# Kernel optimization log

Measured on AMD Instinct MI355X. Metric: run time of the kernel, lower is better.

## Reference

```python
import jax, jax.numpy as jnp
import numpy as np

EPS = 1e-06


def setup_inputs() -> dict:
    key = jax.random.key(0)
    kq, kk, kv = jax.random.split(key, 3)
    shape = (4, 16, 4096, 64)  # [batch, heads, seq, head_dim]
    q = jax.random.normal(kq, shape, dtype=jnp.float32)
    k = jax.random.normal(kk, shape, dtype=jnp.float32)
    v = jax.random.normal(kv, shape, dtype=jnp.float32)
    return {"q": q, "k": k, "v": v}


def reference(q, k, v):
    # elu(x)+1 feature map (positive kernel)
    q_prime = jax.nn.elu(q) + 1.0  # [b,h,s,d]
    k_prime = jax.nn.elu(k) + 1.0  # [b,h,s,d]
    # KV aggregate: [b,h,d,d] -- avoids the [s,s] score matrix
    kv_agg = jnp.einsum('bhsd,bhse->bhde', k_prime, v)
    num = jnp.einsum('bhsd,bhde->bhse', q_prime, kv_agg)  # [b,h,s,d]
    k_sum = k_prime.sum(axis=-2)                           # [b,h,d]
    denom = jnp.einsum('bhsd,bhd->bhs', q_prime, k_sum)[..., None] + EPS
    return num / denom
```

## Files before the change

### kernel.cpp

```cpp
#include <hip/hip_runtime.h>


#define EPS_LA 1e-6f

constexpr int BH = 64;
constexpr int SEQ = 4096;
constexpr int DIM = 64;
constexpr int KVELEM = DIM * DIM + DIM;
constexpr int NPB = 32;
constexpr int SCH = SEQ / NPB;

typedef short bf16x8 __attribute__((ext_vector_type(8)));
typedef float f32x4 __attribute__((ext_vector_type(4)));

__device__ __forceinline__ float elu1(float x) {
    return x > 0.f ? x + 1.f : __expf(x);
}
__device__ __forceinline__ f32x4 elu4v(f32x4 v) {
    v[0] = elu1(v[0]); v[1] = elu1(v[1]); v[2] = elu1(v[2]); v[3] = elu1(v[3]);
    return v;
}
__device__ __forceinline__ f32x4 ntld(const float* p) {
    return __builtin_nontemporal_load((const f32x4*)p);
}
__device__ __forceinline__ void ntst(float* p, f32x4 v) {
    __builtin_nontemporal_store(v, (f32x4*)p);
}

__device__ __forceinline__ unsigned int f2bf(float x) {
    unsigned int u = __float_as_uint(x);
    return (u + 0x7fffu + ((u >> 16) & 1u)) >> 16;
}
__device__ __forceinline__ unsigned int pack2bf(float lo, float hi) {
    return f2bf(lo) | (f2bf(hi) << 16);
}

__device__ __forceinline__ int swz(int d, int s2) {
    return d * 64 + (s2 ^ ((((d >> 1) ^ (d >> 2)) & 7) << 2));
}

template<bool ATOMIC>
__global__ __launch_bounds__(256, 2) void kv_mfma_kernel(
    const float* __restrict__ K, const float* __restrict__ V,
    float* __restrict__ dst) {
    const int bh = blockIdx.y;
    const int blk = blockIdx.x;
    const int t = threadIdx.x;
    const int w = t >> 6, l = t & 63;

    __shared__ unsigned int KT[64 * 64];
    __shared__ unsigned int VT[64 * 64];
    __shared__ float csumS[4][64];

    const float* Kb = K + ((size_t)bh * SEQ + (size_t)blk * SCH) * DIM;
    const float* Vb = V + ((size_t)bh * SEQ + (size_t)blk * SCH) * DIM;

    const int c0 = (t & 15) * 4;
    const int pg = t >> 4;
    const int lg = l >> 4;
    const int lr = l & 15;

    f32x4 kf[8], vf[8];
    #pragma unroll
    for (int i = 0; i < 4; ++i) {
        const int p = pg + 16 * i;
        kf[2 * i]     = ntld(Kb + (size_t)(2 * p) * DIM + c0);
        kf[2 * i + 1] = ntld(Kb + (size_t)(2 * p + 1) * DIM + c0);
    }
    #pragma unroll
    for (int i = 0; i < 4; ++i) {
        const int p = pg + 16 * i;
        vf[2 * i]     = ntld(Vb + (size_t)(2 * p) * DIM + c0);
        vf[2 * i + 1] = ntld(Vb + (size_t)(2 * p + 1) * DIM + c0);
    }

    float cs0 = 0.f, cs1 = 0.f, cs2 = 0.f, cs3 = 0.f;
    #pragma unroll
    for (int i = 0; i < 4; ++i) {
        const int p = pg + 16 * i;
        const f32x4 ka = elu4v(kf[2 * i]);
        const f32x4 kb = elu4v(kf[2 * i + 1]);
        cs0 += ka[0] + kb[0]; cs1 += ka[1] + kb[1];
        cs2 += ka[2] + kb[2]; cs3 += ka[3] + kb[3];
        KT[swz(c0 + 0, p)] = pack2bf(ka[0], kb[0]);
        KT[swz(c0 + 1, p)] = pack2bf(ka[1], kb[1]);
        KT[swz(c0 + 2, p)] = pack2bf(ka[2], kb[2]);
        KT[swz(c0 + 3, p)] = pack2bf(ka[3], kb[3]);
        const f32x4 va = vf[2 * i], vb = vf[2 * i + 1];
        VT[swz(c0 + 0, p)] = pack2bf(va[0], vb[0]);
        VT[swz(c0 + 1, p)] = pack2bf(va[1], vb[1]);
        VT[swz(c0 + 2, p)] = pack2bf(va[2], vb[2]);
        VT[swz(c0 + 3, p)] = pack2bf(va[3], vb[3]);
    }

    cs0 += __shfl_xor(cs0, 16); cs0 += __shfl_xor(cs0, 32);
    cs1 += __shfl_xor(cs1, 16); cs1 += __shfl_xor(cs1, 32);
    cs2 += __shfl_xor(cs2, 16); cs2 += __shfl_xor(cs2, 32);
    cs3 += __shfl_xor(cs3, 16); cs3 += __shfl_xor(cs3, 32);
    if (l < 16) *(f32x4*)&csumS[w][l * 4] = f32x4{cs0, cs1, cs2, cs3};

    __syncthreads();

    f32x4 acc[4];
    #pragma unroll
    for (int m = 0; m < 4; ++m)
        #pragma unroll
        for (int r = 0; r < 4; ++r) acc[m][r] = 0.f;

    #pragma unroll
    for (int ks = 0; ks < 4; ++ks) {
        const int s2b = ks * 16 + lg * 4;
        const bf16x8 bfrag =
            *reinterpret_cast<const bf16x8*>(&VT[swz(16 * w + lr, s2b)]);
        #pragma unroll
        for (int m = 0; m < 4; ++m) {
            const bf16x8 afrag =
                *reinterpret_cast<const bf16x8*>(&KT[swz(16 * m + lr, s2b)]);
            acc[m] = __builtin_amdgcn_mfma_f32_16x16x32_bf16(afrag, bfrag, acc[m],
                                                             0, 0, 0);
        }
    }

    float* wout = ATOMIC ? dst + (size_t)bh * KVELEM
                         : dst + ((size_t)blk * BH + bh) * KVELEM;

    if (t < 64) {
        const float s = csumS[0][t] + csumS[1][t] + csumS[2][t] + csumS[3][t];
        if (ATOMIC) atomicAdd(&wout[DIM * DIM + t], s);
        else        wout[DIM * DIM + t] = s;
    }

    #pragma unroll
    for (int m = 0; m < 4; ++m) {
        #pragma unroll
        for (int r = 0; r < 4; ++r) {
            const int d = 16 * m + 4 * lg + r;
            const int e = 16 * w + lr;
            if (ATOMIC) atomicAdd(&wout[(size_t)d * DIM + e], acc[m][r]);
            else        wout[(size_t)d * DIM + e] = acc[m][r];
        }
    }
}

__global__ __launch_bounds__(256) void reduce_partials_kernel(
    const float* __restrict__ partial, float* __restrict__ fin) {
    const int bh = blockIdx.y;
    const int j = blockIdx.x * 256 + threadIdx.x;
    if (j >= KVELEM) return;
    float s = 0.f;
    #pragma unroll
    for (int c = 0; c < NPB; ++c)
        s += partial[((size_t)c * BH + bh) * KVELEM + j];
    fin[(size_t)bh * KVELEM + j] = s;
}

__global__ __launch_bounds__(256) void out_kernel(
    const float* __restrict__ Q, const float* __restrict__ ws,
    float* __restrict__ out) {
    const int bh = blockIdx.y;
    const int rb = blockIdx.x;
    const int wave = threadIdx.x >> 6, lane = threadIdx.x & 63;
    const int t = threadIdx.x;
    const int tr = lane >> 3;
    const int tc = lane & 7;

    const float* w = ws + (size_t)bh * KVELEM;
    const float* Qw = Q + ((size_t)bh * SEQ + (size_t)rb * 128 + (size_t)wave * 32) * DIM;
    float* Ow = out + ((size_t)bh * SEQ + (size_t)rb * 128 + (size_t)wave * 32) * DIM;

    __shared__ float kvS[DIM][DIM];
    __shared__ float ksumS[DIM];
    __shared__ float qS[4][32][DIM];

    #pragma unroll
    for (int i = 0; i < 4; ++i) {
        const int idx = (i * 256 + t) * 4;
        *(f32x4*)&kvS[idx >> 6][idx & 63] = *(const f32x4*)(w + idx);
    }
    if (t < DIM) ksumS[t] = w[DIM * DIM + t];

    #pragma unroll
    for (int it = 0; it < 8; ++it) {
        const int row = it * 4 + (lane >> 4);
        const int cc = lane & 15;
        const f32x4 qv = elu4v(ntld(Qw + (size_t)row * DIM + cc * 4));
        *(f32x4*)&qS[wave][row][((cc ^ ((row >> 2) & 7)) & 15) * 4] = qv;
    }
    __syncthreads();

    float acc[4][8] = {{0.f}};
    float accd[4] = {0.f, 0.f, 0.f, 0.f};

    #pragma unroll 2
    for (int dc = 0; dc < 16; ++dc) {
        f32x4 qv[4];
        #pragma unroll
        for (int i = 0; i < 4; ++i)
            qv[i] = *(const f32x4*)&qS[wave][tr * 4 + i][((dc ^ tr) & 15) * 4];
        const f32x4 ks = *(const f32x4*)&ksumS[dc * 4];
        #pragma unroll
        for (int dd = 0; dd < 4; ++dd) {
            const int d = dc * 4 + dd;
            const f32x4 ka = *(const f32x4*)&kvS[d][tc * 8];
            const f32x4 kb = *(const f32x4*)&kvS[d][tc * 8 + 4];
            const float ksd = ks[dd];
            #pragma unroll
            for (int i = 0; i < 4; ++i) {
                const float qq = qv[i][dd];
                accd[i] += qq * ksd;
                acc[i][0] += qq * ka[0]; acc[i][1] += qq * ka[1];
                acc[i][2] += qq * ka[2]; acc[i][3] += qq * ka[3];
                acc[i][4] += qq * kb[0]; acc[i][5] += qq * kb[1];
                acc[i][6] += qq * kb[2]; acc[i][7] += qq * kb[3];
            }
        }
    }

    #pragma unroll
    for (int i = 0; i < 4; ++i) {
        const float inv = 1.f / (accd[i] + EPS_LA);
        f32x4 o0, o1;
        o0[0] = acc[i][0] * inv; o0[1] = acc[i][1] * inv;
        o0[2] = acc[i][2] * inv; o0[3] = acc[i][3] * inv;
        o1[0] = acc[i][4] * inv; o1[1] = acc[i][5] * inv;
        o1[2] = acc[i][6] * inv; o1[3] = acc[i][7] * inv;
        float* orow = Ow + (size_t)(tr * 4 + i) * DIM + tc * 8;
        ntst(orow, o0);
        ntst(orow + 4, o1);
    }
}

extern "C" void kernel_launch(void* const* d_in, const int* in_sizes, int n_in,
                              void* d_out, int out_size, void* d_ws, size_t ws_size,
                              hipStream_t stream) {
    const float* q = (const float*)d_in[0];
    const float* k = (const float*)d_in[1];
    const float* v = (const float*)d_in[2];
    float* out = (float*)d_out;
    float* ws = (float*)d_ws;

    const size_t partial_elems = (size_t)NPB * BH * KVELEM;
    const size_t need = (partial_elems + (size_t)BH * KVELEM) * sizeof(float);

    dim3 blk(256);
    const float* fin_ptr;
    if (ws_size >= need) {
        float* partial = ws;
        float* fin = ws + partial_elems;
        hipLaunchKernelGGL((kv_mfma_kernel<false>), dim3(NPB, BH), blk, 0, stream,
                           k, v, partial);
        hipLaunchKernelGGL(reduce_partials_kernel, dim3((KVELEM + 255) / 256, BH),
                           blk, 0, stream, partial, fin);
        fin_ptr = fin;
    } else {
        float* fin = ws;
        hipMemsetAsync(fin, 0, (size_t)BH * KVELEM * sizeof(float), stream);
        hipLaunchKernelGGL((kv_mfma_kernel<true>), dim3(NPB, BH), blk, 0, stream,
                           k, v, fin);
        fin_ptr = fin;
    }
    hipLaunchKernelGGL(out_kernel, dim3(SEQ / 128, BH), blk, 0, stream,
                       q, fin_ptr, out);
}
```

Baseline: 79.20 us.

## Compute output projection with bf16 MFMA instead of FP32 FMA loops

The output kernel now converts elu(Q)+1 and the KV aggregate to packed bf16 in swizzled LDS and computes Q'·KV with 16x16x32 bf16 MFMA instructions instead of scalar FP32 FMAs. The denominator is computed with fp32 dot products during the Q load and reduced across lanes with shuffles. This is meant to cut ALU cost in the output stage. In exchange it gives up precision on the numerator and stores scalar floats rather than vector writes, which may hurt store coalescing.

```diff
diff --git a/kernel.cpp b/kernel.cpp
--- a/kernel.cpp
+++ b/kernel.cpp
@@ -22,9 +22,6 @@
 }
 __device__ __forceinline__ f32x4 ntld(const float* p) {
     return __builtin_nontemporal_load((const f32x4*)p);
-}
-__device__ __forceinline__ void ntst(float* p, f32x4 v) {
-    __builtin_nontemporal_store(v, (f32x4*)p);
 }
 
 __device__ __forceinline__ unsigned int f2bf(float x) {
@@ -159,74 +156,91 @@
     float* __restrict__ out) {
     const int bh = blockIdx.y;
     const int rb = blockIdx.x;
-    const int wave = threadIdx.x >> 6, lane = threadIdx.x & 63;
     const int t = threadIdx.x;
-    const int tr = lane >> 3;
-    const int tc = lane & 7;
-
-    const float* w = ws + (size_t)bh * KVELEM;
-    const float* Qw = Q + ((size_t)bh * SEQ + (size_t)rb * 128 + (size_t)wave * 32) * DIM;
-    float* Ow = out + ((size_t)bh * SEQ + (size_t)rb * 128 + (size_t)wave * 32) * DIM;
-
-    __shared__ float kvS[DIM][DIM];
-    __shared__ float ksumS[DIM];
-    __shared__ float qS[4][32][DIM];
-
-    #pragma unroll
-    for (int i = 0; i < 4; ++i) {
-        const int idx = (i * 256 + t) * 4;
-        *(f32x4*)&kvS[idx >> 6][idx & 63] = *(const f32x4*)(w + idx);
-    }
-    if (t < DIM) ksumS[t] = w[DIM * DIM + t];
-
+    const int wv = t >> 6, l = t & 63;
+    const int lr = l & 15, lg = l >> 4;
+
+    __shared__ unsigned int qA[4 * 32 * 32];
+    __shared__ unsigned int kvT[64 * 32];
+    __shared__ float denomS[128];
+
+    const float* kvp = ws + (size_t)bh * KVELEM;
+    const float* Qb = Q + ((size_t)bh * SEQ + (size_t)rb * 128) * DIM;
+    float* Ob = out + ((size_t)bh * SEQ + (size_t)rb * 128) * DIM;
+
+    #pragma unroll
+    for (int i = 0; i < 2; ++i) {
+        const int p = (t >> 4) + 16 * i;
+        const int e0 = (t & 15) * 4;
+        const f32x4 a = *(const f32x4*)(kvp + (size_t)(2 * p) * DIM + e0);
+        const f32x4 b = *(const f32x4*)(kvp + (size_t)(2 * p + 1) * DIM + e0);
+        #pragma unroll
+        for (int j = 0; j < 4; ++j) {
+            const int e = e0 + j;
+            kvT[e * 32 + (p ^ ((e & 7) << 2))] = pack2bf(a[j], b[j]);
+        }
+    }
+
+    const int c0 = lr * 4;
+    const f32x4 ks4 = *(const f32x4*)(kvp + DIM * DIM + c0);
+    float pd[8];
     #pragma unroll
     for (int it = 0; it < 8; ++it) {
-        const int row = it * 4 + (lane >> 4);
-        const int cc = lane & 15;
-        const f32x4 qv = elu4v(ntld(Qw + (size_t)row * DIM + cc * 4));
-        *(f32x4*)&qS[wave][row][((cc ^ ((row >> 2) & 7)) & 15) * 4] = qv;
+        const int row = it * 4 + lg;
+        const f32x4 qv = elu4v(ntld(Qb + (size_t)(wv * 32 + row) * DIM + c0));
+        pd[it] = qv[0] * ks4[0] + qv[1] * ks4[1] + qv[2] * ks4[2] + qv[3] * ks4[3];
+        uint2 val;
+        val.x = pack2bf(qv[0], qv[1]);
+        val.y = pack2bf(qv[2], qv[3]);
+        *(uint2*)&qA[wv * 1024 + row * 32 + ((2 * lr) ^ ((row & 7) << 2))] = val;
+    }
+    #pragma unroll
+    for (int it = 0; it < 8; ++it) {
+        float v = pd[it];
+        v += __shfl_xor(v, 1); v += __shfl_xor(v, 2);
+        v += __shfl_xor(v, 4); v += __shfl_xor(v, 8);
+        if (lr == 0) denomS[wv * 32 + it * 4 + lg] = v + EPS_LA;
     }
     __syncthreads();
 
-    float acc[4][8] = {{0.f}};
-    float accd[4] = {0.f, 0.f, 0.f, 0.f};
-
-    #pragma unroll 2
-    for (int dc = 0; dc < 16; ++dc) {
-        f32x4 qv[4];
-        #pragma unroll
-        for (int i = 0; i < 4; ++i)
-            qv[i] = *(const f32x4*)&qS[wave][tr * 4 + i][((dc ^ tr) & 15) * 4];
-        const f32x4 ks = *(const f32x4*)&ksumS[dc * 4];
-        #pragma unroll
-        for (int dd = 0; dd < 4; ++dd) {
-            const int d = dc * 4 + dd;
-            const f32x4 ka = *(const f32x4*)&kvS[d][tc * 8];
-            const f32x4 kb = *(const f32x4*)&kvS[d][tc * 8 + 4];
-            const float ksd = ks[dd];
+    f32x4 acc[2][4];
+    #pragma unroll
+    for (int mt = 0; mt < 2; ++mt)
+        #pragma unroll
+        for (int nt = 0; nt < 4; ++nt)
             #pragma unroll
-            for (int i = 0; i < 4; ++i) {
-                const float qq = qv[i][dd];
-                accd[i] += qq * ksd;
-                acc[i][0] += qq * ka[0]; acc[i][1] += qq * ka[1];
-                acc[i][2] += qq * ka[2]; acc[i][3] += qq * ka[3];
-                acc[i][4] += qq * kb[0]; acc[i][5] += qq * kb[1];
-                acc[i][6] += qq * kb[2]; acc[i][7] += qq * kb[3];
+            for (int r = 0; r < 4; ++r) acc[mt][nt][r] = 0.f;
+
+    #pragma unroll
+    for (int ks = 0; ks < 2; ++ks) {
+        const int kd = 4 * lg + 16 * ks;
+        const int am = (lr & 7) << 2;
+        const bf16x8 a0 = *(const bf16x8*)&qA[wv * 1024 + lr * 32 + (kd ^ am)];
+        const bf16x8 a1 = *(const bf16x8*)&qA[wv * 1024 + (16 + lr) * 32 + (kd ^ am)];
+        #pragma unroll
+        for (int nt = 0; nt < 4; ++nt) {
+            const bf16x8 b =
+                *(const bf16x8*)&kvT[(16 * nt + lr) * 32 + (kd ^ am)];
+            acc[0][nt] = __builtin_amdgcn_mfma_f32_16x16x32_bf16(a0, b, acc[0][nt],
+                                                                 0, 0, 0);
+            acc[1][nt] = __builtin_amdgcn_mfma_f32_16x16x32_bf16(a1, b, acc[1][nt],
+                                                                 0, 0, 0);
+        }
+    }
+
+    #pragma unroll
+    for (int mt = 0; mt < 2; ++mt) {
+        #pragma unroll
+        for (int r = 0; r < 4; ++r) {
+            const int row = 16 * mt + 4 * lg + r;
+            const float inv = 1.f / denomS[wv * 32 + row];
+            float* orow = Ob + (size_t)(wv * 32 + row) * DIM;
+            #pragma unroll
+            for (int nt = 0; nt < 4; ++nt) {
+                __builtin_nontemporal_store(acc[mt][nt][r] * inv,
+                                            orow + 16 * nt + lr);
             }
         }
-    }
-
-    #pragma unroll
-    for (int i = 0; i < 4; ++i) {
-        const float inv = 1.f / (accd[i] + EPS_LA);
-        f32x4 o0, o1;
-        o0[0] = acc[i][0] * inv; o0[1] = acc[i][1] * inv;
-        o0[2] = acc[i][2] * inv; o0[3] = acc[i][3] * inv;
-        o1[0] = acc[i][4] * inv; o1[1] = acc[i][5] * inv;
-        o1[2] = acc[i][6] * inv; o1[3] = acc[i][7] * inv;
-        float* orow = Ow + (size_t)(tr * 4 + i) * DIM + tc * 8;
-        ntst(orow, o0);
-        ntst(orow + 4, o1);
     }
 }
 
```

New measurement: 69.74 us. -11.9%, faster.
